# Kernel optimization log

Hardware: AMD Instinct MI355X
Metric: run time of the kernel (lower is better)

The kernel has to match this reference:

```python
import jax, jax.numpy as jnp
import numpy as np

NU, NI, E = 50000, 20000, 400000
IN, HID, OUT = 128, 256, 128
NEG_SLOPE_ATTN = 0.2   # DGL GATConv default
NEG_SLOPE_ACT = 0.01   # F.leaky_relu default
BN_EPS = 1e-5


def setup_inputs() -> dict:
    key = jax.random.key(0)
    ks = jax.random.split(key, 32)
    d = {}
    d["x_user"] = jax.random.normal(ks[0], (NU, IN), jnp.float32)
    d["x_item"] = jax.random.normal(ks[1], (NI, IN), jnp.float32)
    d["eu"] = jax.random.randint(ks[2], (E,), 0, NU, jnp.int32)
    d["ei"] = jax.random.randint(ks[3], (E,), 0, NI, jnp.int32)
    i = 4
    dims = [(IN, 4, 64), (HID, 4, 64), (HID, 4, 64), (HID, 4, 32)]
    for L, (fin, H, dh) in enumerate(dims):
        for rel in ("ui", "iu"):
            d[f"W{L}_{rel}"] = jax.random.normal(ks[i], (fin, H * dh), jnp.float32) * 0.1; i += 1
            d[f"A{L}_{rel}"] = jax.random.normal(ks[i], (2, H, dh), jnp.float32) * 0.1; i += 1
    # BN params: [layer, (gamma,beta), HID]; gamma near 1, beta near 0
    gu = 1.0 + 0.05 * jax.random.normal(ks[i], (3, 1, HID), jnp.float32); i += 1
    bu = 0.05 * jax.random.normal(ks[i], (3, 1, HID), jnp.float32); i += 1
    gi = 1.0 + 0.05 * jax.random.normal(ks[i], (3, 1, HID), jnp.float32); i += 1
    bi = 0.05 * jax.random.normal(ks[i], (3, 1, HID), jnp.float32); i += 1
    d["bn_u"] = jnp.concatenate([gu, bu], axis=1)
    d["bn_i"] = jnp.concatenate([gi, bi], axis=1)
    return d


def _gat(x_src, x_dst, W, A, src, dst, n_dst):
    # Single-relation bipartite GATConv (DGL semantics).
    H, dh = A.shape[1], A.shape[2]
    hs = (x_src @ W).reshape(-1, H, dh)           # [Ns,H,dh]
    hd = (x_dst @ W).reshape(-1, H, dh)           # [Nd,H,dh]
    el = jnp.einsum('nhd,hd->nh', hs, A[0])
    er = jnp.einsum('nhd,hd->nh', hd, A[1])
    e = jax.nn.leaky_relu(el[src] + er[dst], NEG_SLOPE_ATTN)   # [E,H]
    emax = jax.ops.segment_max(e, dst, num_segments=n_dst)
    ee = jnp.exp(e - emax[dst])
    denom = jax.ops.segment_sum(ee, dst, num_segments=n_dst)
    alpha = ee / denom[dst]                       # segment softmax over in-edges
    out = jax.ops.segment_sum(hs[src] * alpha[..., None], dst, num_segments=n_dst)
    return out.reshape(n_dst, H * dh)


def _bn(x, gamma, beta):
    mu = x.mean(axis=0)
    var = x.var(axis=0)   # biased, matches torch BN normalization
    return gamma * (x - mu) * jax.lax.rsqrt(var + BN_EPS) + beta


def reference(x_user, x_item, eu, ei, W0_ui, W0_iu, A0_ui, A0_iu,
              W1_ui, W1_iu, A1_ui, A1_iu, W2_ui, W2_iu, A2_ui, A2_iu,
              W3_ui, W3_iu, A3_ui, A3_iu, bn_u, bn_i):
    Wui = [W0_ui, W1_ui, W2_ui]; Aui = [A0_ui, A1_ui, A2_ui]
    Wiu = [W0_iu, W1_iu, W2_iu]; Aiu = [A0_iu, A1_iu, A2_iu]
    hu, hi = x_user, x_item
    for L in range(3):
        ni = _gat(hu, hi, Wui[L], Aui[L], eu, ei, NI)   # user -> item
        nu = _gat(hi, hu, Wiu[L], Aiu[L], ei, eu, NU)   # item -> user
        nu = _bn(nu, bn_u[L, 0], bn_u[L, 1])
        ni = _bn(ni, bn_i[L, 0], bn_i[L, 1])
        if L == 2:   # last hidden layer uses tanh in non-residual path
            hu, hi = jnp.tanh(nu), jnp.tanh(ni)
        else:
            hu = jax.nn.leaky_relu(nu, NEG_SLOPE_ACT)
            hi = jax.nn.leaky_relu(ni, NEG_SLOPE_ACT)
    out_i = _gat(hu, hi, W3_ui, A3_ui, eu, ei, NI)
    out_u = _gat(hi, hu, W3_iu, A3_iu, ei, eu, NU)
    return jnp.concatenate([out_u, out_i], axis=0)   # [NU+NI, OUT]
```

## Files before the change

### kernel.cpp

```cpp
#include <hip/hip_runtime.h>

#define NUSERS 50000
#define NITEMS 20000
#define NEDGES 400000

typedef _Float16 f16;
typedef __attribute__((ext_vector_type(8))) _Float16 f16x8;
typedef __attribute__((ext_vector_type(4))) _Float16 f16x4;
typedef __attribute__((ext_vector_type(2))) _Float16 f16x2;
typedef __attribute__((ext_vector_type(4))) float f32x4;

__global__ void prep_k(const float* __restrict__ Wa, const float* __restrict__ Aa,
                       f16* __restrict__ Bta, float* __restrict__ efa,
                       const float* __restrict__ Wb, const float* __restrict__ Ab,
                       f16* __restrict__ Btb, float* __restrict__ efb,
                       int K, int Nw, int dh) {
  int t = blockIdx.x * blockDim.x + threadIdx.x;
  int half = K * Nw;
  if (t >= 2 * half) return;
  const float* W = (t < half) ? Wa : Wb;
  const float* A = (t < half) ? Aa : Ab;
  f16* Bt = (t < half) ? Bta : Btb;
  float* ef = (t < half) ? efa : efb;
  int t2 = (t < half) ? t : t - half;
  int n = t2 / K, k = t2 - n * K;
  Bt[t2] = (f16)W[(long)k * Nw + n];
  if (t2 < K * 8) {
    int j = t2 / (K * 4);
    int r = t2 - j * K * 4;
    int h = r / K, f = r - h * K;
    const float* Aj = A + j * Nw;
    float s = 0.f;
    for (int d = 0; d < dh; ++d) s += W[f * Nw + h * dh + d] * Aj[h * dh + d];
    ef[j * 4 * K + h * K + f] = s;
  }
}

__global__ void xcvt_k(const float* __restrict__ xu, f16* __restrict__ yu, long nu,
                       const float* __restrict__ xi, f16* __restrict__ yi, long ni) {
  long i = (long)blockIdx.x * blockDim.x + threadIdx.x;
  if (i < nu) yu[i] = (f16)xu[i];
  else if (i < nu + ni) yi[i - nu] = (f16)xi[i - nu];
}

__global__ __launch_bounds__(256) void hgemm2_k(const f16* __restrict__ Aa, const f16* __restrict__ Bta,
                                                f16* __restrict__ Ca, int Ma, int gya,
                                                const f16* __restrict__ Ab, const f16* __restrict__ Btb,
                                                f16* __restrict__ Cb, int Mb,
                                                int N, int K) {
  __shared__ f16 As[128 * 32];
  __shared__ f16 Bs[128 * 32];
  int by = blockIdx.y;
  const f16* A; const f16* Bt; f16* C; int M; int row0;
  if (by < gya) { A = Aa; Bt = Bta; C = Ca; M = Ma; row0 = by * 128; }
  else          { A = Ab; Bt = Btb; C = Cb; M = Mb; row0 = (by - gya) * 128; }
  int tid = threadIdx.x;
  int col0 = blockIdx.x * 128;
  int lane = tid & 63, wv = tid >> 6;
  int wr = (wv & 1) * 64, wc = (wv >> 1) * 64;
  int l16 = lane & 15, q = lane >> 4;
  f32x4 acc[4][4] = {};
  int r = tid >> 2, c8 = (tid & 3) * 8;
  for (int k0 = 0; k0 < K; k0 += 32) {
    int ra = min(row0 + r, M - 1);
    uint4 va = *(const uint4*)&A[(long)ra * K + k0 + c8];
    int ra2 = min(row0 + r + 64, M - 1);
    uint4 va2 = *(const uint4*)&A[(long)ra2 * K + k0 + c8];
    uint4 vb = *(const uint4*)&Bt[(long)(col0 + r) * K + k0 + c8];
    uint4 vb2 = *(const uint4*)&Bt[(long)(col0 + r + 64) * K + k0 + c8];
    *(uint4*)&As[r * 32 + c8] = va;
    *(uint4*)&As[(r + 64) * 32 + c8] = va2;
    *(uint4*)&Bs[r * 32 + c8] = vb;
    *(uint4*)&Bs[(r + 64) * 32 + c8] = vb2;
    __syncthreads();
    f16x8 af[4], bfr[4];
#pragma unroll
    for (int i = 0; i < 4; ++i) {
      af[i] = *(const f16x8*)&As[(wr + i * 16 + l16) * 32 + q * 8];
      bfr[i] = *(const f16x8*)&Bs[(wc + i * 16 + l16) * 32 + q * 8];
    }
#pragma unroll
    for (int i = 0; i < 4; ++i)
#pragma unroll
      for (int j = 0; j < 4; ++j)
        acc[i][j] = __builtin_amdgcn_mfma_f32_16x16x32_f16(af[i], bfr[j], acc[i][j], 0, 0, 0);
    __syncthreads();
  }
#pragma unroll
  for (int i = 0; i < 4; ++i) {
#pragma unroll
    for (int reg = 0; reg < 4; ++reg) {
      int rr = row0 + wr + i * 16 + q * 4 + reg;
      if (rr < M) {
#pragma unroll
        for (int j = 0; j < 4; ++j)
          C[(long)rr * N + col0 + wc + j * 16 + l16] = (f16)acc[i][j][reg];
      }
    }
  }
}

__global__ __launch_bounds__(256) void eler_k(
    const f16* __restrict__ hbu, const float* __restrict__ ef_ui, const float* __restrict__ ef_iu,
    float* __restrict__ el_u, float* __restrict__ er_u,
    const f16* __restrict__ hbi, float* __restrict__ el_i, float* __restrict__ er_i, int K) {
  __shared__ float xs[256];
  int b = blockIdx.x, t = threadIdx.x;
  const f16* hb; const float* elf; const float* erf; float* el; float* er; int n;
  if (b < NUSERS) { hb = hbu; elf = ef_ui; erf = ef_iu + 4 * K; el = el_u; er = er_u; n = b; }
  else            { hb = hbi; elf = ef_iu; erf = ef_ui + 4 * K; el = el_i; er = er_i; n = b - NUSERS; }
  if (t < K) xs[t] = (float)hb[(long)n * K + t];
  __syncthreads();
  int j = t >> 5, l = t & 31;
  const float* fr = (j < 4) ? (elf + j * K) : (erf + (j - 4) * K);
  float p = 0.f;
  for (int f = l; f < K; f += 32) p += xs[f] * fr[f];
#pragma unroll
  for (int off = 16; off; off >>= 1) p += __shfl_down(p, off, 32);
  if (l == 0) { if (j < 4) el[n * 4 + j] = p; else er[n * 4 + (j - 4)] = p; }
}

__global__ void hist_k(const int* __restrict__ ei, int* __restrict__ degi,
                       const int* __restrict__ eu, int* __restrict__ degu) {
  int e = blockIdx.x * blockDim.x + threadIdx.x;
  if (e < NEDGES) atomicAdd(&degi[ei[e]], 1);
  else if (e < 2 * NEDGES) atomicAdd(&degu[eu[e - NEDGES]], 1);
}

__global__ __launch_bounds__(256) void scan1_k(const int* __restrict__ deg,
                                               int* __restrict__ bsum, int N) {
  __shared__ int red[256];
  int base = blockIdx.x * 1024, t = threadIdx.x;
  int s = 0;
#pragma unroll
  for (int j = 0; j < 4; ++j) { int i = base + t * 4 + j; s += (i < N) ? deg[i] : 0; }
  red[t] = s; __syncthreads();
  for (int off = 128; off; off >>= 1) { if (t < off) red[t] += red[t + off]; __syncthreads(); }
  if (t == 0) bsum[blockIdx.x] = red[0];
}

__global__ void scan2_k(int* __restrict__ bsum, int nb) {
  if (threadIdx.x == 0) {
    int run = 0;
    for (int i = 0; i < nb; ++i) { int v = bsum[i]; bsum[i] = run; run += v; }
  }
}

__global__ __launch_bounds__(256) void scan3_k(const int* __restrict__ deg,
                                               const int* __restrict__ bsum,
                                               int* __restrict__ rowptr, int N) {
  __shared__ int tsum[256];
  int base = blockIdx.x * 1024, t = threadIdx.x;
  int v[4]; int s = 0;
#pragma unroll
  for (int j = 0; j < 4; ++j) { int i = base + t * 4 + j; v[j] = (i < N) ? deg[i] : 0; s += v[j]; }
  tsum[t] = s; __syncthreads();
  for (int off = 1; off < 256; off <<= 1) {
    int x = (t >= off) ? tsum[t - off] : 0;
    __syncthreads();
    tsum[t] += x;
    __syncthreads();
  }
  int run = bsum[blockIdx.x] + ((t > 0) ? tsum[t - 1] : 0);
#pragma unroll
  for (int j = 0; j < 4; ++j) {
    int i = base + t * 4 + j;
    if (i < N) rowptr[i] = run;
    run += v[j];
  }
}

__global__ void setval_k(int* __restrict__ p, int v) { *p = v; }

__global__ void copy2_k(const int* __restrict__ a, int* __restrict__ b, int Na,
                        const int* __restrict__ c, int* __restrict__ d, int Nc) {
  int i = blockIdx.x * blockDim.x + threadIdx.x;
  if (i < Na) b[i] = a[i];
  else if (i < Na + Nc) d[i - Na] = c[i - Na];
}

__global__ void scat_k(const int* __restrict__ ei, const int* __restrict__ eu,
                       int* __restrict__ curi, int* __restrict__ srci,
                       int* __restrict__ curu, int* __restrict__ srcu) {
  int e = blockIdx.x * blockDim.x + threadIdx.x;
  if (e < NEDGES) {
    int p = atomicAdd(&curi[ei[e]], 1);
    srci[p] = eu[e];
  } else if (e < 2 * NEDGES) {
    int e2 = e - NEDGES;
    int p = atomicAdd(&curu[eu[e2]], 1);
    srcu[p] = ei[e2];
  }
}

template <int W, int DH, typename OUT>
__global__ __launch_bounds__(256) void agg_k(
    const float* __restrict__ elA, const float* __restrict__ erA,
    const int* __restrict__ rpA, const int* __restrict__ srcA,
    const f16* __restrict__ hsA, OUT* __restrict__ outA, int nA,
    const float* __restrict__ elB, const float* __restrict__ erB,
    const int* __restrict__ rpB, const int* __restrict__ srcB,
    const f16* __restrict__ hsB, OUT* __restrict__ outB, int nB) {
  constexpr int CPL = W >> 6;
  constexpr int SHIFT = (W == 256) ? 9 : 8;
  constexpr bool OF16 = (sizeof(OUT) == 2);
  __shared__ float alds[4][256];
  __shared__ int soff[4][64];
  int wv = threadIdx.x >> 6;
  int g = blockIdx.x * 4 + wv;
  int lane = threadIdx.x & 63;
  const float* el; const float* er; const int* rp; const int* srcv;
  const f16* hs; OUT* outp; int d;
  if (g < nA)           { el = elA; er = erA; rp = rpA; srcv = srcA; hs = hsA; outp = outA; d = g; }
  else if (g < nA + nB) { el = elB; er = erB; rp = rpB; srcv = srcB; hs = hsB; outp = outB; d = g - nA; }
  else return;
  int s0 = rp[d], s1 = rp[d + 1];
  int deg = s1 - s0;
  int c0 = lane * CPL;
  int h = c0 / DH;
  long obase = (long)d * W + c0;
  if (deg == 0) {
#pragma unroll
    for (int q = 0; q < CPL; ++q) outp[obase + q] = (OUT)0.f;
    return;
  }
  const float NEG = -3.0e38f;
  float acc[CPL];
#pragma unroll
  for (int q = 0; q < CPL; ++q) acc[q] = 0.f;
  float inv;

  if (deg <= 64) {
    int hh = lane & 3, p = lane >> 2;
    float er_h = er[d * 4 + hh];
    float vv[4];
    float vmax = NEG;
#pragma unroll
    for (int j = 0; j < 4; ++j) {
      int slot = j * 16 + p;
      vv[j] = NEG;
      if (slot < deg) {
        int sj = srcv[s0 + slot];
        if (hh == 0) soff[wv][slot] = sj << SHIFT;
        float v = el[sj * 4 + hh] + er_h;
        v = v > 0.f ? v : 0.2f * v;
        vv[j] = v;
        vmax = fmaxf(vmax, v);
      }
    }
#pragma unroll
    for (int off = 4; off < 64; off <<= 1) vmax = fmaxf(vmax, __shfl_xor(vmax, off, 64));
    float ssum = 0.f;
#pragma unroll
    for (int j = 0; j < 4; ++j) {
      int slot = j * 16 + p;
      if (slot < deg) {
        float e = expf(vv[j] - vmax);
        alds[wv][slot * 4 + hh] = e;
        ssum += e;
      } else {
        alds[wv][slot * 4 + hh] = 0.f;
        if (hh == 0) soff[wv][slot] = 0;
      }
    }
#pragma unroll
    for (int off = 4; off < 64; off <<= 1) ssum += __shfl_xor(ssum, off, 64);
    float Sh = __shfl(ssum, (lane & ~3) | h, 64);
    inv = 1.0f / Sh;
    const char* hbase = (const char*)hs + (size_t)c0 * sizeof(f16);
    int degp = (deg + 3) & ~3;
    for (int j = 0; j < degp; j += 4) {
      float aj[4]; int oj[4];
#pragma unroll
      for (int u = 0; u < 4; ++u) {
        aj[u] = alds[wv][(j + u) * 4 + h];
        oj[u] = soff[wv][j + u];
      }
      if constexpr (CPL == 4) {
        f16x4 vj[4];
#pragma unroll
        for (int u = 0; u < 4; ++u)
          vj[u] = *(const f16x4*)(hbase + (size_t)(unsigned)oj[u]);
#pragma unroll
        for (int u = 0; u < 4; ++u) {
          acc[0] += aj[u] * (float)vj[u][0];
          acc[1] += aj[u] * (float)vj[u][1];
          acc[2] += aj[u] * (float)vj[u][2];
          acc[3] += aj[u] * (float)vj[u][3];
        }
      } else {
        f16x2 vj[4];
#pragma unroll
        for (int u = 0; u < 4; ++u)
          vj[u] = *(const f16x2*)(hbase + (size_t)(unsigned)oj[u]);
#pragma unroll
        for (int u = 0; u < 4; ++u) {
          acc[0] += aj[u] * (float)vj[u][0];
          acc[1] += aj[u] * (float)vj[u][1];
        }
      }
    }
  } else {
    float4 er4 = *(const float4*)&er[d * 4];
    float m0 = NEG, m1 = NEG, m2 = NEG, m3 = NEG;
    for (int k = s0 + lane; k < s1; k += 64) {
      int s = srcv[k];
      float4 e4 = *(const float4*)&el[s * 4];
      float v;
      v = e4.x + er4.x; v = v > 0.f ? v : 0.2f * v; m0 = fmaxf(m0, v);
      v = e4.y + er4.y; v = v > 0.f ? v : 0.2f * v; m1 = fmaxf(m1, v);
      v = e4.z + er4.z; v = v > 0.f ? v : 0.2f * v; m2 = fmaxf(m2, v);
      v = e4.w + er4.w; v = v > 0.f ? v : 0.2f * v; m3 = fmaxf(m3, v);
    }
#pragma unroll
    for (int off = 32; off; off >>= 1) {
      m0 = fmaxf(m0, __shfl_xor(m0, off, 64));
      m1 = fmaxf(m1, __shfl_xor(m1, off, 64));
      m2 = fmaxf(m2, __shfl_xor(m2, off, 64));
      m3 = fmaxf(m3, __shfl_xor(m3, off, 64));
    }
    float S0 = 0.f, S1 = 0.f, S2 = 0.f, S3 = 0.f;
    for (int k = s0 + lane; k < s1; k += 64) {
      int s = srcv[k];
      float4 e4 = *(const float4*)&el[s * 4];
      float v;
      v = e4.x + er4.x; v = v > 0.f ? v : 0.2f * v; S0 += expf(v - m0);
      v = e4.y + er4.y; v = v > 0.f ? v : 0.2f * v; S1 += expf(v - m1);
      v = e4.z + er4.z; v = v > 0.f ? v : 0.2f * v; S2 += expf(v - m2);
      v = e4.w + er4.w; v = v > 0.f ? v : 0.2f * v; S3 += expf(v - m3);
    }
#pragma unroll
    for (int off = 32; off; off >>= 1) {
      S0 += __shfl_xor(S0, off, 64);
      S1 += __shfl_xor(S1, off, 64);
      S2 += __shfl_xor(S2, off, 64);
      S3 += __shfl_xor(S3, off, 64);
    }
    float mh = h == 0 ? m0 : h == 1 ? m1 : h == 2 ? m2 : m3;
    float Sh = h == 0 ? S0 : h == 1 ? S1 : h == 2 ? S2 : S3;
    float erh = h == 0 ? er4.x : h == 1 ? er4.y : h == 2 ? er4.z : er4.w;
    inv = 1.0f / Sh;
    for (int k = s0; k < s1; ++k) {
      int s = srcv[k];
      float v = el[s * 4 + h] + erh; v = v > 0.f ? v : 0.2f * v;
      float a = expf(v - mh);
      const f16* row = &hs[(long)s * W + c0];
      if constexpr (CPL == 4) {
        f16x4 hv = *(const f16x4*)row;
        acc[0] += a * (float)hv[0]; acc[1] += a * (float)hv[1];
        acc[2] += a * (float)hv[2]; acc[3] += a * (float)hv[3];
      } else {
        f16x2 hv = *(const f16x2*)row;
        acc[0] += a * (float)hv[0]; acc[1] += a * (float)hv[1];
      }
    }
  }
  if constexpr (OF16) {
    if constexpr (CPL == 4) {
      f16x4 o = { (f16)(acc[0] * inv), (f16)(acc[1] * inv), (f16)(acc[2] * inv), (f16)(acc[3] * inv) };
      *(f16x4*)&outp[obase] = o;
    } else {
      f16x2 o = { (f16)(acc[0] * inv), (f16)(acc[1] * inv) };
      *(f16x2*)&outp[obase] = o;
    }
  } else {
    if constexpr (CPL == 4) {
      *(float4*)&outp[obase] = make_float4(acc[0] * inv, acc[1] * inv, acc[2] * inv, acc[3] * inv);
    } else {
      *(float2*)&outp[obase] = make_float2(acc[0] * inv, acc[1] * inv);
    }
  }
}

__global__ void zero2_k(float* __restrict__ a, float* __restrict__ b) {
  int t = threadIdx.x;
  a[t] = 0.f; b[t] = 0.f;
}

__global__ __launch_bounds__(256) void bn_stats2_k(const f16* __restrict__ xu, float* __restrict__ su, int Nu, int gU,
                                                   const f16* __restrict__ xi, float* __restrict__ si, int Ni) {
  const int C = 256;
  int b = blockIdx.x;
  const f16* x; float* sums; int N; int r0;
  if (b < gU) { x = xu; sums = su; N = Nu; r0 = b * 64; }
  else        { x = xi; sums = si; N = Ni; r0 = (b - gU) * 64; }
  int c = threadIdx.x;
  int r1 = min(r0 + 64, N);
  float s = 0.f, s2 = 0.f;
  for (int r = r0; r < r1; ++r) {
    float v = (float)x[(long)r * C + c];
    s += v; s2 += v * v;
  }
  atomicAdd(&sums[c], s);
  atomicAdd(&sums[C + c], s2);
}

__global__ __launch_bounds__(256) void bn_fused_k(
    const f16* __restrict__ xu, const float* __restrict__ su, const float* __restrict__ gbu,
    f16* __restrict__ yu, int Nu,
    const f16* __restrict__ xi, const float* __restrict__ si, const float* __restrict__ gbi,
    f16* __restrict__ yi, int Ni,
    const float* __restrict__ efu, const float* __restrict__ efiu,
    float* __restrict__ el_u, float* __restrict__ er_u,
    float* __restrict__ el_i, float* __restrict__ er_i, int act) {
  const int Kn = 256;
  __shared__ float xs[256];
  int b = blockIdx.x, t = threadIdx.x;
  const f16* x; const float* sums; const float* gb; f16* y; int n; int N;
  const float* elf; const float* erf; float* el; float* er;
  if (b < Nu) { x = xu; sums = su; gb = gbu; y = yu; n = b; N = Nu; elf = efu;  erf = efiu + 4 * Kn; el = el_u; er = er_u; }
  else        { x = xi; sums = si; gb = gbi; y = yi; n = b - Nu; N = Ni; elf = efiu; erf = efu + 4 * Kn;  el = el_i; er = er_i; }
  long base = (long)n * 256;
  float val = (float)x[base + t];
  float inv_n = 1.0f / (float)N;
  float mean = sums[t] * inv_n;
  float var = sums[256 + t] * inv_n - mean * mean;
  float v = gb[t] * (val - mean) * rsqrtf(var + 1e-5f) + gb[256 + t];
  v = act ? tanhf(v) : (v > 0.f ? v : 0.01f * v);
  y[base + t] = (f16)v;
  xs[t] = v;
  __syncthreads();
  int j = t >> 5, l = t & 31;
  const float* fr = (j < 4) ? (elf + j * Kn) : (erf + (j - 4) * Kn);
  float p = 0.f;
  for (int f = l; f < Kn; f += 32) p += xs[f] * fr[f];
#pragma unroll
  for (int off = 16; off; off >>= 1) p += __shfl_down(p, off, 32);
  if (l == 0) { if (j < 4) el[n * 4 + j] = p; else er[n * 4 + (j - 4)] = p; }
}

extern "C" void kernel_launch(void* const* d_in, const int* in_sizes, int n_in,
                              void* d_out, int out_size, void* d_ws, size_t ws_size,
                              hipStream_t stream) {
  const float* x_user = (const float*)d_in[0];
  const float* x_item = (const float*)d_in[1];
  const int* eu = (const int*)d_in[2];
  const int* ei = (const int*)d_in[3];
  const float *Wm[4][2], *Am[4][2];
  for (int L = 0; L < 4; ++L) {
    Wm[L][0] = (const float*)d_in[4 + L * 4 + 0];
    Am[L][0] = (const float*)d_in[4 + L * 4 + 1];
    Wm[L][1] = (const float*)d_in[4 + L * 4 + 2];
    Am[L][1] = (const float*)d_in[4 + L * 4 + 3];
  }
  const float* bnu = (const float*)d_in[20];
  const float* bni = (const float*)d_in[21];
  float* out = (float*)d_out;

  float* ws = (float*)d_ws;
  size_t o = 0;
  float* el_u = ws + o; o += (size_t)NUSERS * 4;
  float* er_u = ws + o; o += (size_t)NUSERS * 4;
  float* el_i = ws + o; o += (size_t)NITEMS * 4;
  float* er_i = ws + o; o += (size_t)NITEMS * 4;
  float* ef_all[4][2];
  for (int L = 0; L < 4; ++L)
    for (int rl = 0; rl < 2; ++rl) { ef_all[L][rl] = ws + o; o += 2048; }
  float* bns_u = ws + o; o += 512;
  float* bns_i = ws + o; o += 512;
  f16* hb_u   = (f16*)(ws + o); o += (size_t)NUSERS * 128;
  f16* hb_i   = (f16*)(ws + o); o += (size_t)NITEMS * 128;
  f16* hsb_u  = (f16*)(ws + o); o += (size_t)NUSERS * 128;
  f16* hsb_i  = (f16*)(ws + o); o += (size_t)NITEMS * 128;
  f16* aggh_u = (f16*)(ws + o); o += (size_t)NUSERS * 128;
  f16* aggh_i = (f16*)(ws + o); o += (size_t)NITEMS * 128;
  f16* Bt_all[4][2];
  for (int L = 0; L < 4; ++L) {
    int K = (L == 0) ? 128 : 256;
    int W = (L == 3) ? 128 : 256;
    for (int rl = 0; rl < 2; ++rl) { Bt_all[L][rl] = (f16*)(ws + o); o += (size_t)K * W / 2; }
  }
  int* deg_i    = (int*)(ws + o); o += NITEMS;
  int* deg_u    = (int*)(ws + o); o += NUSERS;
  int* rowptr_i = (int*)(ws + o); o += NITEMS + 1;
  int* rowptr_u = (int*)(ws + o); o += NUSERS + 1;
  int* cur_i    = (int*)(ws + o); o += NITEMS;
  int* cur_u    = (int*)(ws + o); o += NUSERS;
  int* bsum     = (int*)(ws + o); o += 256;
  int* csrsrc_i = (int*)(ws + o); o += NEDGES;
  int* csrsrc_u = (int*)(ws + o); o += NEDGES;

  const int gE2 = (2 * NEDGES + 255) / 256;
  const int nb_i = (NITEMS + 1023) / 1024;
  const int nb_u = (NUSERS + 1023) / 1024;
  const int gU = (NUSERS + 63) / 64;
  const int gI = (NITEMS + 63) / 64;

  hipMemsetAsync(deg_i, 0, (NITEMS + NUSERS) * sizeof(int), stream);
  hist_k<<<dim3(gE2), dim3(256), 0, stream>>>(ei, deg_i, eu, deg_u);
  scan1_k<<<dim3(nb_i), dim3(256), 0, stream>>>(deg_i, bsum, NITEMS);
  scan2_k<<<dim3(1), dim3(64), 0, stream>>>(bsum, nb_i);
  scan3_k<<<dim3(nb_i), dim3(256), 0, stream>>>(deg_i, bsum, rowptr_i, NITEMS);
  setval_k<<<dim3(1), dim3(1), 0, stream>>>(rowptr_i + NITEMS, NEDGES);
  scan1_k<<<dim3(nb_u), dim3(256), 0, stream>>>(deg_u, bsum, NUSERS);
  scan2_k<<<dim3(1), dim3(64), 0, stream>>>(bsum, nb_u);
  scan3_k<<<dim3(nb_u), dim3(256), 0, stream>>>(deg_u, bsum, rowptr_u, NUSERS);
  setval_k<<<dim3(1), dim3(1), 0, stream>>>(rowptr_u + NUSERS, NEDGES);
  copy2_k<<<dim3((NITEMS + NUSERS + 255) / 256), dim3(256), 0, stream>>>(rowptr_i, cur_i, NITEMS, rowptr_u, cur_u, NUSERS);
  scat_k<<<dim3(gE2), dim3(256), 0, stream>>>(ei, eu, cur_i, csrsrc_i, cur_u, csrsrc_u);

  for (int L = 0; L < 4; ++L) {
    int K = (L == 0) ? 128 : 256;
    int dh = (L == 3) ? 32 : 64;
    int W = 4 * dh;
    prep_k<<<dim3((2 * K * W + 255) / 256), dim3(256), 0, stream>>>(
        Wm[L][0], Am[L][0], Bt_all[L][0], ef_all[L][0],
        Wm[L][1], Am[L][1], Bt_all[L][1], ef_all[L][1], K, W, dh);
  }

  xcvt_k<<<dim3(((NUSERS + NITEMS) * 128 + 255) / 256), dim3(256), 0, stream>>>(
      x_user, hb_u, (long)NUSERS * 128, x_item, hb_i, (long)NITEMS * 128);
  eler_k<<<dim3(NUSERS + NITEMS), dim3(256), 0, stream>>>(
      hb_u, ef_all[0][0], ef_all[0][1], el_u, er_u, hb_i, el_i, er_i, 128);

  int K = 128;
  for (int L = 0; L < 4; ++L) {
    const int dh = (L == 3) ? 32 : 64;
    const int W = 4 * dh;

    const int gya = (NUSERS + 127) / 128, gyb = (NITEMS + 127) / 128;
    hgemm2_k<<<dim3(W / 128, gya + gyb), dim3(256), 0, stream>>>(
        hb_u, Bt_all[L][0], hsb_u, NUSERS, gya, hb_i, Bt_all[L][1], hsb_i, NITEMS, W, K);

    const int gAgg = (NITEMS + NUSERS + 3) / 4;
    if (L < 3) {
      agg_k<256, 64, f16><<<dim3(gAgg), dim3(256), 0, stream>>>(
          el_u, er_i, rowptr_i, csrsrc_i, hsb_u, aggh_i, NITEMS,
          el_i, er_u, rowptr_u, csrsrc_u, hsb_i, aggh_u, NUSERS);
      zero2_k<<<dim3(1), dim3(512), 0, stream>>>(bns_u, bns_i);
      bn_stats2_k<<<dim3(gU + gI), dim3(256), 0, stream>>>(aggh_u, bns_u, NUSERS, gU, aggh_i, bns_i, NITEMS);
      bn_fused_k<<<dim3(NUSERS + NITEMS), dim3(256), 0, stream>>>(
          aggh_u, bns_u, bnu + L * 512, hb_u, NUSERS,
          aggh_i, bns_i, bni + L * 512, hb_i, NITEMS,
          ef_all[L + 1][0], ef_all[L + 1][1],
          el_u, er_u, el_i, er_i, L == 2);
      K = 256;
    } else {
      agg_k<128, 32, float><<<dim3(gAgg), dim3(256), 0, stream>>>(
          el_u, er_i, rowptr_i, csrsrc_i, hsb_u, out + (size_t)NUSERS * 128, NITEMS,
          el_i, er_u, rowptr_u, csrsrc_u, hsb_i, out, NUSERS);
    }
  }
}
```

Baseline: 910.0 us.

## Widen GEMM tile to full output width and use nontemporal aggregation stores

The feature GEMM is templated on the output tile width so that one block computes all 256 (or 128) output columns for its 128 rows. Each A tile is then loaded once instead of once per column block, at the cost of more accumulator registers and a larger B shared-memory tile. The aggregation kernel's output writes become nontemporal stores so they do not evict cached gather data. The CSR buffers also get small padding.

```diff
diff --git a/kernel.cpp b/kernel.cpp
--- a/kernel.cpp
+++ b/kernel.cpp
@@ -9,6 +9,7 @@
 typedef __attribute__((ext_vector_type(4))) _Float16 f16x4;
 typedef __attribute__((ext_vector_type(2))) _Float16 f16x2;
 typedef __attribute__((ext_vector_type(4))) float f32x4;
+typedef __attribute__((ext_vector_type(2))) float f32x2;
 
 __global__ void prep_k(const float* __restrict__ Wa, const float* __restrict__ Aa,
                        f16* __restrict__ Bta, float* __restrict__ efa,
@@ -43,46 +44,52 @@
   else if (i < nu + ni) yi[i - nu] = (f16)xi[i - nu];
 }
 
-__global__ __launch_bounds__(256) void hgemm2_k(const f16* __restrict__ Aa, const f16* __restrict__ Bta,
-                                                f16* __restrict__ Ca, int Ma, int gya,
-                                                const f16* __restrict__ Ab, const f16* __restrict__ Btb,
-                                                f16* __restrict__ Cb, int Mb,
-                                                int N, int K) {
+template <int NTILE>
+__global__ __launch_bounds__(256) void hgemm_k(const f16* __restrict__ Aa, const f16* __restrict__ Bta,
+                                               f16* __restrict__ Ca, int Ma, int gya,
+                                               const f16* __restrict__ Ab, const f16* __restrict__ Btb,
+                                               f16* __restrict__ Cb, int Mb, int K) {
+  constexpr int JN = NTILE / 32;
+  constexpr int WC = NTILE / 2;
+  constexpr int NB = NTILE / 64;
   __shared__ f16 As[128 * 32];
-  __shared__ f16 Bs[128 * 32];
-  int by = blockIdx.y;
+  __shared__ f16 Bs[NTILE * 32];
+  int by = blockIdx.x;
   const f16* A; const f16* Bt; f16* C; int M; int row0;
   if (by < gya) { A = Aa; Bt = Bta; C = Ca; M = Ma; row0 = by * 128; }
   else          { A = Ab; Bt = Btb; C = Cb; M = Mb; row0 = (by - gya) * 128; }
   int tid = threadIdx.x;
-  int col0 = blockIdx.x * 128;
   int lane = tid & 63, wv = tid >> 6;
-  int wr = (wv & 1) * 64, wc = (wv >> 1) * 64;
+  int wr = (wv & 1) * 64, wc = (wv >> 1) * WC;
   int l16 = lane & 15, q = lane >> 4;
-  f32x4 acc[4][4] = {};
+  f32x4 acc[4][JN] = {};
   int r = tid >> 2, c8 = (tid & 3) * 8;
   for (int k0 = 0; k0 < K; k0 += 32) {
     int ra = min(row0 + r, M - 1);
     uint4 va = *(const uint4*)&A[(long)ra * K + k0 + c8];
     int ra2 = min(row0 + r + 64, M - 1);
     uint4 va2 = *(const uint4*)&A[(long)ra2 * K + k0 + c8];
-    uint4 vb = *(const uint4*)&Bt[(long)(col0 + r) * K + k0 + c8];
-    uint4 vb2 = *(const uint4*)&Bt[(long)(col0 + r + 64) * K + k0 + c8];
+    uint4 vb[NB];
+#pragma unroll
+    for (int c = 0; c < NB; ++c)
+      vb[c] = *(const uint4*)&Bt[(long)(c * 64 + r) * K + k0 + c8];
     *(uint4*)&As[r * 32 + c8] = va;
     *(uint4*)&As[(r + 64) * 32 + c8] = va2;
-    *(uint4*)&Bs[r * 32 + c8] = vb;
-    *(uint4*)&Bs[(r + 64) * 32 + c8] = vb2;
+#pragma unroll
+    for (int c = 0; c < NB; ++c)
+      *(uint4*)&Bs[(c * 64 + r) * 32 + c8] = vb[c];
     __syncthreads();
-    f16x8 af[4], bfr[4];
-#pragma unroll
-    for (int i = 0; i < 4; ++i) {
+    f16x8 af[4], bfr[JN];
+#pragma unroll
+    for (int i = 0; i < 4; ++i)
       af[i] = *(const f16x8*)&As[(wr + i * 16 + l16) * 32 + q * 8];
-      bfr[i] = *(const f16x8*)&Bs[(wc + i * 16 + l16) * 32 + q * 8];
-    }
+#pragma unroll
+    for (int j = 0; j < JN; ++j)
+      bfr[j] = *(const f16x8*)&Bs[(wc + j * 16 + l16) * 32 + q * 8];
 #pragma unroll
     for (int i = 0; i < 4; ++i)
 #pragma unroll
-      for (int j = 0; j < 4; ++j)
+      for (int j = 0; j < JN; ++j)
         acc[i][j] = __builtin_amdgcn_mfma_f32_16x16x32_f16(af[i], bfr[j], acc[i][j], 0, 0, 0);
     __syncthreads();
   }
@@ -93,8 +100,8 @@
       int rr = row0 + wr + i * 16 + q * 4 + reg;
       if (rr < M) {
 #pragma unroll
-        for (int j = 0; j < 4; ++j)
-          C[(long)rr * N + col0 + wc + j * 16 + l16] = (f16)acc[i][j][reg];
+        for (int j = 0; j < JN; ++j)
+          C[(long)rr * NTILE + wc + j * 16 + l16] = (f16)acc[i][j][reg];
       }
     }
   }
@@ -358,16 +365,18 @@
   if constexpr (OF16) {
     if constexpr (CPL == 4) {
       f16x4 o = { (f16)(acc[0] * inv), (f16)(acc[1] * inv), (f16)(acc[2] * inv), (f16)(acc[3] * inv) };
-      *(f16x4*)&outp[obase] = o;
+      __builtin_nontemporal_store(o, (f16x4*)&outp[obase]);
     } else {
       f16x2 o = { (f16)(acc[0] * inv), (f16)(acc[1] * inv) };
-      *(f16x2*)&outp[obase] = o;
+      __builtin_nontemporal_store(o, (f16x2*)&outp[obase]);
     }
   } else {
     if constexpr (CPL == 4) {
-      *(float4*)&outp[obase] = make_float4(acc[0] * inv, acc[1] * inv, acc[2] * inv, acc[3] * inv);
+      f32x4 o = { acc[0] * inv, acc[1] * inv, acc[2] * inv, acc[3] * inv };
+      __builtin_nontemporal_store(o, (f32x4*)&outp[obase]);
     } else {
-      *(float2*)&outp[obase] = make_float2(acc[0] * inv, acc[1] * inv);
+      f32x2 o = { acc[0] * inv, acc[1] * inv };
+      __builtin_nontemporal_store(o, (f32x2*)&outp[obase]);
     }
   }
 }
@@ -472,13 +481,13 @@
   }
   int* deg_i    = (int*)(ws + o); o += NITEMS;
   int* deg_u    = (int*)(ws + o); o += NUSERS;
-  int* rowptr_i = (int*)(ws + o); o += NITEMS + 1;
-  int* rowptr_u = (int*)(ws + o); o += NUSERS + 1;
+  int* rowptr_i = (int*)(ws + o); o += NITEMS + 4;
+  int* rowptr_u = (int*)(ws + o); o += NUSERS + 4;
   int* cur_i    = (int*)(ws + o); o += NITEMS;
   int* cur_u    = (int*)(ws + o); o += NUSERS;
   int* bsum     = (int*)(ws + o); o += 256;
-  int* csrsrc_i = (int*)(ws + o); o += NEDGES;
-  int* csrsrc_u = (int*)(ws + o); o += NEDGES;
+  int* csrsrc_i = (int*)(ws + o); o += NEDGES + 4;
+  int* csrsrc_u = (int*)(ws + o); o += NEDGES + 4;
 
   const int gE2 = (2 * NEDGES + 255) / 256;
   const int nb_i = (NITEMS + 1023) / 1024;
@@ -514,16 +523,12 @@
       hb_u, ef_all[0][0], ef_all[0][1], el_u, er_u, hb_i, el_i, er_i, 128);
 
   int K = 128;
+  const int gAgg = (NITEMS + NUSERS + 3) / 4;
+  const int gya = (NUSERS + 127) / 128, gyb = (NITEMS + 127) / 128;
   for (int L = 0; L < 4; ++L) {
-    const int dh = (L == 3) ? 32 : 64;
-    const int W = 4 * dh;
-
-    const int gya = (NUSERS + 127) / 128, gyb = (NITEMS + 127) / 128;
-    hgemm2_k<<<dim3(W / 128, gya + gyb), dim3(256), 0, stream>>>(
-        hb_u, Bt_all[L][0], hsb_u, NUSERS, gya, hb_i, Bt_all[L][1], hsb_i, NITEMS, W, K);
-
-    const int gAgg = (NITEMS + NUSERS + 3) / 4;
     if (L < 3) {
+      hgemm_k<256><<<dim3(gya + gyb), dim3(256), 0, stream>>>(
+          hb_u, Bt_all[L][0], hsb_u, NUSERS, gya, hb_i, Bt_all[L][1], hsb_i, NITEMS, K);
       agg_k<256, 64, f16><<<dim3(gAgg), dim3(256), 0, stream>>>(
           el_u, er_i, rowptr_i, csrsrc_i, hsb_u, aggh_i, NITEMS,
           el_i, er_u, rowptr_u, csrsrc_u, hsb_i, aggh_u, NUSERS);
@@ -536,6 +541,8 @@
           el_u, er_u, el_i, er_i, L == 2);
       K = 256;
     } else {
+      hgemm_k<128><<<dim3(gya + gyb), dim3(256), 0, stream>>>(
+          hb_u, Bt_all[L][0], hsb_u, NUSERS, gya, hb_i, Bt_all[L][1], hsb_i, NITEMS, K);
       agg_k<128, 32, float><<<dim3(gAgg), dim3(256), 0, stream>>>(
           el_u, er_i, rowptr_i, csrsrc_i, hsb_u, out + (size_t)NUSERS * 128, NITEMS,
           el_i, er_u, rowptr_u, csrsrc_u, hsb_i, out, NUSERS);
```

After: 971.2 us. 6.7% more time.
